# Optimization experiments

Measured on AMD Instinct MI355X. Metric: run time of the kernel, lower is better.

The kernel has to match this reference:

```python
import jax, jax.numpy as jnp
import numpy as np
import math

S, E = 4096, 2048
H = 4 * E  # FFN hidden
EPS = 1e-5


def _ln_all(y):
    # F.layer_norm(y, y.shape): normalize over ALL elements, no affine
    mu = jnp.mean(y)
    var = jnp.mean(jnp.square(y - mu))
    return (y - mu) / jnp.sqrt(var + EPS)


def setup_inputs() -> dict:
    key = jax.random.key(0)
    ks = jax.random.split(key, 12)
    sc = 0.02
    return {
        "x": jax.random.normal(ks[0], (S, E), dtype=jnp.float32),
        "Wq": jax.random.normal(ks[1], (E, E), dtype=jnp.float32) * sc,
        "bq": jnp.zeros((E,), dtype=jnp.float32),
        "Wk": jax.random.normal(ks[2], (E, E), dtype=jnp.float32) * sc,
        "bk": jnp.zeros((E,), dtype=jnp.float32),
        "Wv": jax.random.normal(ks[3], (E, E), dtype=jnp.float32) * sc,
        "bv": jnp.zeros((E,), dtype=jnp.float32),
        "W1": jax.random.normal(ks[4], (E, H), dtype=jnp.float32) * sc,
        "b1": jnp.zeros((H,), dtype=jnp.float32),
        "W2": jax.random.normal(ks[5], (H, E), dtype=jnp.float32) * sc,
        "b2": jnp.zeros((E,), dtype=jnp.float32),
    }


def reference(x, Wq, bq, Wk, bk, Wv, bv, W1, b1, W2, b2):
    # projections
    Q = x @ Wq + bq  # [S, E]
    K = x @ Wk + bk
    V = x @ Wv + bv
    # NOTE: source scales by sqrt(K.size(-2)) == sqrt(seq_len), not head dim
    scale = 1.0 / math.sqrt(x.shape[-2])
    scores = jax.nn.softmax((Q @ K.T) * scale, axis=-1)  # [S, S]
    attn = scores @ V  # [S, E]
    h = _ln_all(x + attn)
    ffn = jax.nn.relu(h @ W1 + b1) @ W2 + b2
    return _ln_all(h + ffn)
```

## Files before the change

kernel.cpp:

```cpp
#include <hip/hip_runtime.h>
#include <cstdint>
#include <cstddef>


constexpr int S = 4096;
constexpr int E = 2048;
constexpr int H = 8192;

typedef __bf16 bf16;
typedef bf16  bf16x8 __attribute__((ext_vector_type(8)));
typedef bf16  bf16x4 __attribute__((ext_vector_type(4)));
typedef float f32x4  __attribute__((ext_vector_type(4)));

typedef __attribute__((address_space(1))) void as1_void;
typedef __attribute__((address_space(3))) void as3_void;

__device__ __forceinline__ void ldg2lds16(const void* g, void* l) {
  __builtin_amdgcn_global_load_lds((as1_void*)g, (as3_void*)l, 16, 0, 0);
}

template <int EPI>
__global__ __launch_bounds__(256, 3)
void gemm_bt(const bf16* __restrict__ A, int lda,
             const bf16* __restrict__ Bt, int ldb,
             bf16* __restrict__ Cb, float* __restrict__ Cf, int ldc,
             const float* __restrict__ bias, const float* __restrict__ add,
             const bf16* __restrict__ addb,
             float* __restrict__ red, int M, int N, int K, float scale)
{
  __shared__ bf16 sA[128 * 64];
  __shared__ bf16 sB[128 * 64];

  const int tid  = threadIdx.x;
  const int lane = tid & 63;
  const int wave = tid >> 6;

  const int ntiles = gridDim.x;
  const int b      = blockIdx.y * ntiles + blockIdx.x;
  const int group  = b >> 6;
  const int within = b & 63;
  const int gpr    = ntiles >> 3;
  const int m0 = ((group / gpr) * 8 + (within >> 3)) * 128;
  const int n0 = ((group % gpr) * 8 + (within & 7)) * 128;

  const int wm = (wave & 1) * 64;
  const int wn = (wave >> 1) * 64;

  const int sr = tid >> 3;
  const int gsw = ((tid & 7) ^ (sr & 7)) * 8;
  const bf16* gA = A  + (size_t)(m0 + sr) * lda + gsw;
  const bf16* gB = Bt + (size_t)(n0 + sr) * ldb + gsw;
  const size_t a32 = (size_t)32 * lda;
  const size_t b32 = (size_t)32 * ldb;
  bf16* lA = &sA[tid * 8];
  bf16* lB = &sB[tid * 8];

  const int fr = lane & 15;
  const int fq = lane >> 4;
  const int p0 = (fq ^ (fr & 7)) * 8;
  const int p1 = p0 ^ 32;
  const bf16* rA = &sA[(wm + fr) * 64];
  const bf16* rB = &sB[(wn + fr) * 64];

  f32x4 acc[4][4] = {};

  for (int k0 = 0; k0 < K; k0 += 64) {
    ldg2lds16(gA,           lA);
    ldg2lds16(gA +     a32, lA + 32 * 64);
    ldg2lds16(gA + 2 * a32, lA + 64 * 64);
    ldg2lds16(gA + 3 * a32, lA + 96 * 64);
    ldg2lds16(gB,           lB);
    ldg2lds16(gB +     b32, lB + 32 * 64);
    ldg2lds16(gB + 2 * b32, lB + 64 * 64);
    ldg2lds16(gB + 3 * b32, lB + 96 * 64);
    gA += 64; gB += 64;
    __syncthreads();

    bf16x8 a0[4], a1[4], b0[4], b1[4];
#pragma unroll
    for (int i = 0; i < 4; ++i) {
      a0[i] = *(const bf16x8*)(rA + i * 1024 + p0);
      a1[i] = *(const bf16x8*)(rA + i * 1024 + p1);
    }
#pragma unroll
    for (int j = 0; j < 4; ++j) {
      b0[j] = *(const bf16x8*)(rB + j * 1024 + p0);
      b1[j] = *(const bf16x8*)(rB + j * 1024 + p1);
    }
#pragma unroll
    for (int i = 0; i < 4; ++i)
#pragma unroll
      for (int j = 0; j < 4; ++j)
        acc[i][j] = __builtin_amdgcn_mfma_f32_16x16x32_bf16(a0[i], b0[j], acc[i][j], 0, 0, 0);
#pragma unroll
    for (int i = 0; i < 4; ++i)
#pragma unroll
      for (int j = 0; j < 4; ++j)
        acc[i][j] = __builtin_amdgcn_mfma_f32_16x16x32_bf16(a1[i], b1[j], acc[i][j], 0, 0, 0);
    __syncthreads();
  }

  const int er = m0 + wm + fq * 4;
  const int ec = n0 + wn + fr;
  float ls = 0.f, ls2 = 0.f;
#pragma unroll
  for (int i = 0; i < 4; ++i) {
#pragma unroll
    for (int r = 0; r < 4; ++r) {
      const int gr = er + i * 16 + r;
#pragma unroll
      for (int j = 0; j < 4; ++j) {
        const int gc = ec + j * 16;
        const size_t idx = (size_t)gr * ldc + gc;
        float v = acc[i][j][r];
        if (EPI == 0) {
          v += bias[gc];
          Cb[idx] = (bf16)v;
        } else if (EPI == 1) {
          v += bias[gr];
          Cb[idx] = (bf16)v;
        } else if (EPI == 2) {
          Cb[idx] = (bf16)(v * scale);
        } else if (EPI == 3) {
          v += add[idx];
          Cf[idx] = v; ls += v; ls2 += v * v;
        } else if (EPI == 4) {
          v += bias[gc];
          v = v > 0.f ? v : 0.f;
          Cb[idx] = (bf16)v;
        } else {
          v += bias[gc] + (float)addb[idx];
          Cf[idx] = v; ls += v; ls2 += v * v;
        }
      }
    }
  }

  if (EPI == 3 || EPI == 5) {
#pragma unroll
    for (int o = 32; o; o >>= 1) {
      ls  += __shfl_xor(ls,  o, 64);
      ls2 += __shfl_xor(ls2, o, 64);
    }
    float* sred = (float*)sA;
    if (lane == 0) { sred[wave * 2] = ls; sred[wave * 2 + 1] = ls2; }
    __syncthreads();
    if (tid == 0) {
      atomicAdd(red,     sred[0] + sred[2] + sred[4] + sred[6]);
      atomicAdd(red + 1, sred[1] + sred[3] + sred[5] + sred[7]);
    }
  }
}

__global__ __launch_bounds__(256)
void cvt_f32_bf16(const float* __restrict__ src, bf16* __restrict__ dst)
{
  const size_t i = ((size_t)blockIdx.x * 256 + threadIdx.x) * 4;
  const float4 t = *(const float4*)(src + i);
  bf16x4 b;
  b[0] = (bf16)t.x; b[1] = (bf16)t.y; b[2] = (bf16)t.z; b[3] = (bf16)t.w;
  *(bf16x4*)(dst + i) = b;
}

__global__ __launch_bounds__(256)
void transpose_cvt(const float* __restrict__ src, bf16* __restrict__ dst, int R, int C)
{
  __shared__ float tile[32][33];
  const int c0 = blockIdx.x * 32, r0 = blockIdx.y * 32;
  const int tx = threadIdx.x & 31, ty = threadIdx.x >> 5;
#pragma unroll
  for (int rr = ty; rr < 32; rr += 8)
    tile[rr][tx] = src[(size_t)(r0 + rr) * C + (c0 + tx)];
  __syncthreads();
#pragma unroll
  for (int rr = ty; rr < 32; rr += 8)
    dst[(size_t)(c0 + rr) * R + (r0 + tx)] = (bf16)tile[tx][rr];
}

__global__ __launch_bounds__(256)
void softmax_rows(bf16* __restrict__ P)
{
  const int row  = blockIdx.x;
  bf16* p = P + (size_t)row * 4096;
  const int tid  = threadIdx.x;
  const int lane = tid & 63, wave = tid >> 6;

  bf16x8 c0 = *(const bf16x8*)(p + tid * 16);
  bf16x8 c1 = *(const bf16x8*)(p + tid * 16 + 8);
  float v[16];
#pragma unroll
  for (int i = 0; i < 8; ++i) { v[i] = (float)c0[i]; v[8 + i] = (float)c1[i]; }

  float m = v[0];
#pragma unroll
  for (int i = 1; i < 16; ++i) m = fmaxf(m, v[i]);
#pragma unroll
  for (int o = 32; o; o >>= 1) m = fmaxf(m, __shfl_xor(m, o, 64));
  __shared__ float sred[8];
  if (lane == 0) sred[wave] = m;
  __syncthreads();
  m = fmaxf(fmaxf(sred[0], sred[1]), fmaxf(sred[2], sred[3]));

  float s = 0.f;
#pragma unroll
  for (int i = 0; i < 16; ++i) { v[i] = __expf(v[i] - m); s += v[i]; }
#pragma unroll
  for (int o = 32; o; o >>= 1) s += __shfl_xor(s, o, 64);
  if (lane == 0) sred[4 + wave] = s;
  __syncthreads();
  s = sred[4] + sred[5] + sred[6] + sred[7];

  const float inv = 1.f / s;
  bf16x8 o0, o1;
#pragma unroll
  for (int i = 0; i < 8; ++i) { o0[i] = (bf16)(v[i] * inv); o1[i] = (bf16)(v[8 + i] * inv); }
  *(bf16x8*)(p + tid * 16)     = o0;
  *(bf16x8*)(p + tid * 16 + 8) = o1;
}

__global__ void ln_finalize(float* red, float n)
{
  const float mu  = red[0] / n;
  const float var = red[1] / n - mu * mu;
  red[2] = mu;
  red[3] = rsqrtf(var + 1e-5f);
}

__global__ __launch_bounds__(256)
void ln_apply(const float* __restrict__ y, const float* __restrict__ red,
              float* __restrict__ of, bf16* __restrict__ ob)
{
  const float mu = red[2], rs = red[3];
  const size_t i = ((size_t)blockIdx.x * 256 + threadIdx.x) * 4;
  float4 t = *(const float4*)(y + i);
  t.x = (t.x - mu) * rs; t.y = (t.y - mu) * rs;
  t.z = (t.z - mu) * rs; t.w = (t.w - mu) * rs;
  if (of) *(float4*)(of + i) = t;
  if (ob) {
    bf16x4 b;
    b[0] = (bf16)t.x; b[1] = (bf16)t.y; b[2] = (bf16)t.z; b[3] = (bf16)t.w;
    *(bf16x4*)(ob + i) = b;
  }
}

extern "C" void kernel_launch(void* const* d_in, const int* in_sizes, int n_in,
                              void* d_out, int out_size, void* d_ws, size_t ws_size,
                              hipStream_t stream)
{
  const float* x  = (const float*)d_in[0];
  const float* Wq = (const float*)d_in[1];
  const float* bq = (const float*)d_in[2];
  const float* Wk = (const float*)d_in[3];
  const float* bk = (const float*)d_in[4];
  const float* Wv = (const float*)d_in[5];
  const float* bv = (const float*)d_in[6];
  const float* W1 = (const float*)d_in[7];
  const float* b1 = (const float*)d_in[8];
  const float* W2 = (const float*)d_in[9];
  const float* b2 = (const float*)d_in[10];
  float* out = (float*)d_out;

  const size_t MB = 1ull << 20;
  char* ws = (char*)d_ws;

  bf16*  xb  = (bf16*)(ws);
  bf16*  hb  = xb;
  bf16*  WqT = (bf16*)(ws + 16 * MB);
  bf16*  WkT = (bf16*)(ws + 24 * MB);
  bf16*  WvT = (bf16*)(ws + 32 * MB);
  bf16*  W1T = (bf16*)(ws + 40 * MB);
  bf16*  W2T = (bf16*)(ws + 72 * MB);
  bf16*  Qb  = (bf16*)(ws + 104 * MB);
  bf16*  Kb  = (bf16*)(ws + 120 * MB);
  bf16*  Pb  = (bf16*)(ws + 136 * MB);
  bf16*  act = (bf16*)(ws + 104 * MB);
  bf16*  VbT = (bf16*)(ws + 168 * MB);
  float* y   = (float*)(ws + 184 * MB);
  float* red = (float*)(ws + 216 * MB);

  hipMemsetAsync(red, 0, 32, stream);

  const dim3 blk(256);
  const int nElemBlocks = (S * E) / 1024;

  cvt_f32_bf16<<<dim3(nElemBlocks), blk, 0, stream>>>(x, xb);
  transpose_cvt<<<dim3(E / 32, E / 32), blk, 0, stream>>>(Wq, WqT, E, E);
  transpose_cvt<<<dim3(E / 32, E / 32), blk, 0, stream>>>(Wk, WkT, E, E);
  transpose_cvt<<<dim3(E / 32, E / 32), blk, 0, stream>>>(Wv, WvT, E, E);
  transpose_cvt<<<dim3(H / 32, E / 32), blk, 0, stream>>>(W1, W1T, E, H);
  transpose_cvt<<<dim3(E / 32, H / 32), blk, 0, stream>>>(W2, W2T, H, E);

  gemm_bt<0><<<dim3(E / 128, S / 128), blk, 0, stream>>>(
      xb, E, WqT, E, Qb, nullptr, E, bq, nullptr, nullptr, nullptr, S, E, E, 0.f);
  gemm_bt<0><<<dim3(E / 128, S / 128), blk, 0, stream>>>(
      xb, E, WkT, E, Kb, nullptr, E, bk, nullptr, nullptr, nullptr, S, E, E, 0.f);
  gemm_bt<1><<<dim3(S / 128, E / 128), blk, 0, stream>>>(
      WvT, E, xb, E, VbT, nullptr, S, bv, nullptr, nullptr, nullptr, E, S, E, 0.f);

  gemm_bt<2><<<dim3(S / 128, S / 128), blk, 0, stream>>>(
      Qb, E, Kb, E, Pb, nullptr, S, nullptr, nullptr, nullptr, nullptr, S, S, E, 1.0f / 64.0f);
  softmax_rows<<<dim3(S), blk, 0, stream>>>(Pb);

  gemm_bt<3><<<dim3(E / 128, S / 128), blk, 0, stream>>>(
      Pb, S, VbT, S, nullptr, y, E, nullptr, x, nullptr, red, S, E, S, 0.f);
  ln_finalize<<<1, 1, 0, stream>>>(red, (float)((size_t)S * E));
  ln_apply<<<dim3(nElemBlocks), blk, 0, stream>>>(y, red, nullptr, hb);

  gemm_bt<4><<<dim3(H / 128, S / 128), blk, 0, stream>>>(
      hb, E, W1T, E, act, nullptr, H, b1, nullptr, nullptr, nullptr, S, H, E, 0.f);

  gemm_bt<5><<<dim3(E / 128, S / 128), blk, 0, stream>>>(
      act, H, W2T, H, nullptr, y, E, b2, nullptr, hb, red + 4, S, E, H, 0.f);
  ln_finalize<<<1, 1, 0, stream>>>(red + 4, (float)((size_t)S * E));
  ln_apply<<<dim3(nElemBlocks), blk, 0, stream>>>(y, red + 4, out, nullptr);
}
```

Baseline: 861.3 us.

## Replace GEMM with 8-wave 128x256 double-buffered pipelined kernel

Rewrites the bf16 GEMM used for all projections, attention, and FFN as a 512-thread, 128x256-tile kernel with double-buffered LDS. Global-to-LDS prefetches of the next K-slice are interleaved with four MFMA phases, using manual waitcnt, barriers and s_setprio. A new workgroup-to-tile remapping spreads consecutive block IDs. The aim is to hide global load latency and improve operand reuse. In exchange it uses more LDS and relies on fragile hand-placed synchronization.

New measurement: 1.005 ms. +16.7%, slower.

```diff
diff --git a/kernel.cpp b/kernel.cpp
--- a/kernel.cpp
+++ b/kernel.cpp
@@ -20,84 +20,151 @@
 }
 
 template <int EPI>
-__global__ __launch_bounds__(256, 3)
-void gemm_bt(const bf16* __restrict__ A, int lda,
-             const bf16* __restrict__ Bt, int ldb,
-             bf16* __restrict__ Cb, float* __restrict__ Cf, int ldc,
-             const float* __restrict__ bias, const float* __restrict__ add,
-             const bf16* __restrict__ addb,
-             float* __restrict__ red, int M, int N, int K, float scale)
-{
-  __shared__ bf16 sA[128 * 64];
-  __shared__ bf16 sB[128 * 64];
+__global__ __launch_bounds__(512, 2)
+void gemm8(const bf16* __restrict__ A, int lda,
+           const bf16* __restrict__ Bt, int ldb,
+           bf16* __restrict__ Cb, float* __restrict__ Cf, int ldc,
+           const float* __restrict__ bias, const float* __restrict__ add,
+           const bf16* __restrict__ addb,
+           float* __restrict__ red, int M, int N, int K, float scale)
+{
+  __shared__ bf16 sA[2][128 * 64];
+  __shared__ bf16 sB[2][256 * 64];
 
   const int tid  = threadIdx.x;
   const int lane = tid & 63;
   const int wave = tid >> 6;
 
-  const int ntiles = gridDim.x;
-  const int b      = blockIdx.y * ntiles + blockIdx.x;
-  const int group  = b >> 6;
-  const int within = b & 63;
-  const int gpr    = ntiles >> 3;
-  const int m0 = ((group / gpr) * 8 + (within >> 3)) * 128;
-  const int n0 = ((group % gpr) * 8 + (within & 7)) * 128;
+  const int nbx = gridDim.x;
+  const int nwg = nbx * gridDim.y;
+  const int bid = blockIdx.y * nbx + blockIdx.x;
+  const int wg  = (bid & 7) * (nwg >> 3) + (bid >> 3);
+  const int m0  = (wg / nbx) * 128;
+  const int n0  = (wg % nbx) * 256;
 
   const int wm = (wave & 1) * 64;
   const int wn = (wave >> 1) * 64;
 
-  const int sr = tid >> 3;
-  const int gsw = ((tid & 7) ^ (sr & 7)) * 8;
-  const bf16* gA = A  + (size_t)(m0 + sr) * lda + gsw;
-  const bf16* gB = Bt + (size_t)(n0 + sr) * ldb + gsw;
-  const size_t a32 = (size_t)32 * lda;
-  const size_t b32 = (size_t)32 * ldb;
-  bf16* lA = &sA[tid * 8];
-  bf16* lB = &sB[tid * 8];
+  const int tr  = tid >> 3;
+  const int tc  = tid & 7;
+  const int gsw = (tc ^ (tr & 7)) * 8;
+  const bf16* gA = A  + (size_t)(m0 + tr) * lda + gsw;
+  const bf16* gB = Bt + (size_t)(n0 + tr) * ldb + gsw;
+  const size_t a64 = (size_t)64 * lda;
+  const size_t b64 = (size_t)64 * ldb;
 
   const int fr = lane & 15;
   const int fq = lane >> 4;
   const int p0 = (fq ^ (fr & 7)) * 8;
   const int p1 = p0 ^ 32;
-  const bf16* rA = &sA[(wm + fr) * 64];
-  const bf16* rB = &sB[(wn + fr) * 64];
+
+  const int NT = K >> 6;
+
+  ldg2lds16(gA,             &sA[0][tid * 8]);
+  ldg2lds16(gA + a64,       &sA[0][4096  + tid * 8]);
+  ldg2lds16(gB,             &sB[0][tid * 8]);
+  ldg2lds16(gB + b64,       &sB[0][4096  + tid * 8]);
+  ldg2lds16(gB + 2 * b64,   &sB[0][8192  + tid * 8]);
+  ldg2lds16(gB + 3 * b64,   &sB[0][12288 + tid * 8]);
+  ldg2lds16(gA + 64,        &sA[1][tid * 8]);
+  ldg2lds16(gA + 64 + a64,  &sA[1][4096  + tid * 8]);
+  asm volatile("s_waitcnt vmcnt(2)" ::: "memory");
+  __builtin_amdgcn_s_barrier();
 
   f32x4 acc[4][4] = {};
 
-  for (int k0 = 0; k0 < K; k0 += 64) {
-    ldg2lds16(gA,           lA);
-    ldg2lds16(gA +     a32, lA + 32 * 64);
-    ldg2lds16(gA + 2 * a32, lA + 64 * 64);
-    ldg2lds16(gA + 3 * a32, lA + 96 * 64);
-    ldg2lds16(gB,           lB);
-    ldg2lds16(gB +     b32, lB + 32 * 64);
-    ldg2lds16(gB + 2 * b32, lB + 64 * 64);
-    ldg2lds16(gB + 3 * b32, lB + 96 * 64);
-    gA += 64; gB += 64;
-    __syncthreads();
-
-    bf16x8 a0[4], a1[4], b0[4], b1[4];
-#pragma unroll
-    for (int i = 0; i < 4; ++i) {
-      a0[i] = *(const bf16x8*)(rA + i * 1024 + p0);
-      a1[i] = *(const bf16x8*)(rA + i * 1024 + p1);
-    }
-#pragma unroll
-    for (int j = 0; j < 4; ++j) {
-      b0[j] = *(const bf16x8*)(rB + j * 1024 + p0);
-      b1[j] = *(const bf16x8*)(rB + j * 1024 + p1);
-    }
-#pragma unroll
-    for (int i = 0; i < 4; ++i)
-#pragma unroll
-      for (int j = 0; j < 4; ++j)
-        acc[i][j] = __builtin_amdgcn_mfma_f32_16x16x32_bf16(a0[i], b0[j], acc[i][j], 0, 0, 0);
-#pragma unroll
-    for (int i = 0; i < 4; ++i)
-#pragma unroll
-      for (int j = 0; j < 4; ++j)
-        acc[i][j] = __builtin_amdgcn_mfma_f32_16x16x32_bf16(a1[i], b1[j], acc[i][j], 0, 0, 0);
-    __syncthreads();
+  for (int t = 0; t < NT; ++t) {
+    const int bu = t & 1, nx = bu ^ 1;
+    const bf16* rA = &sA[bu][(wm + fr) * 64];
+    const bf16* rB = &sB[bu][(wn + fr) * 64];
+    bf16x8 aF0[2], aF1[2], bF0[4], bF1[4];
+
+    aF0[0] = *(const bf16x8*)(rA + p0);
+    aF1[0] = *(const bf16x8*)(rA + p1);
+    aF0[1] = *(const bf16x8*)(rA + 1024 + p0);
+    aF1[1] = *(const bf16x8*)(rA + 1024 + p1);
+    bF0[0] = *(const bf16x8*)(rB + p0);
+    bF1[0] = *(const bf16x8*)(rB + p1);
+    bF0[1] = *(const bf16x8*)(rB + 1024 + p0);
+    bF1[1] = *(const bf16x8*)(rB + 1024 + p1);
+    if (t + 1 < NT) {
+      const bf16* g = gB + ((size_t)(t + 1) << 6);
+      ldg2lds16(g,       &sB[nx][tid * 8]);
+      ldg2lds16(g + b64, &sB[nx][4096 + tid * 8]);
+    }
+    __builtin_amdgcn_s_barrier();
+    asm volatile("s_waitcnt lgkmcnt(0)" ::: "memory");
+    __builtin_amdgcn_s_setprio(1);
+#pragma unroll
+    for (int i = 0; i < 2; ++i)
+#pragma unroll
+      for (int j = 0; j < 2; ++j) {
+        acc[i][j] = __builtin_amdgcn_mfma_f32_16x16x32_bf16(aF0[i], bF0[j], acc[i][j], 0, 0, 0);
+        acc[i][j] = __builtin_amdgcn_mfma_f32_16x16x32_bf16(aF1[i], bF1[j], acc[i][j], 0, 0, 0);
+      }
+    __builtin_amdgcn_s_setprio(0);
+    __builtin_amdgcn_s_barrier();
+
+    bF0[2] = *(const bf16x8*)(rB + 2048 + p0);
+    bF1[2] = *(const bf16x8*)(rB + 2048 + p1);
+    bF0[3] = *(const bf16x8*)(rB + 3072 + p0);
+    bF1[3] = *(const bf16x8*)(rB + 3072 + p1);
+    if (t + 1 < NT) {
+      const bf16* g = gB + ((size_t)(t + 1) << 6) + 2 * b64;
+      ldg2lds16(g,       &sB[nx][8192  + tid * 8]);
+      ldg2lds16(g + b64, &sB[nx][12288 + tid * 8]);
+    }
+    __builtin_amdgcn_s_barrier();
+    asm volatile("s_waitcnt lgkmcnt(0)" ::: "memory");
+    __builtin_amdgcn_s_setprio(1);
+#pragma unroll
+    for (int i = 0; i < 2; ++i)
+#pragma unroll
+      for (int j = 0; j < 2; ++j) {
+        acc[i][2 + j] = __builtin_amdgcn_mfma_f32_16x16x32_bf16(aF0[i], bF0[2 + j], acc[i][2 + j], 0, 0, 0);
+        acc[i][2 + j] = __builtin_amdgcn_mfma_f32_16x16x32_bf16(aF1[i], bF1[2 + j], acc[i][2 + j], 0, 0, 0);
+      }
+    __builtin_amdgcn_s_setprio(0);
+    __builtin_amdgcn_s_barrier();
+
+    aF0[0] = *(const bf16x8*)(rA + 2048 + p0);
+    aF1[0] = *(const bf16x8*)(rA + 2048 + p1);
+    aF0[1] = *(const bf16x8*)(rA + 3072 + p0);
+    aF1[1] = *(const bf16x8*)(rA + 3072 + p1);
+    __builtin_amdgcn_s_barrier();
+    asm volatile("s_waitcnt lgkmcnt(0)" ::: "memory");
+    __builtin_amdgcn_s_setprio(1);
+#pragma unroll
+    for (int i = 0; i < 2; ++i)
+#pragma unroll
+      for (int j = 0; j < 2; ++j) {
+        acc[2 + i][j] = __builtin_amdgcn_mfma_f32_16x16x32_bf16(aF0[i], bF0[j], acc[2 + i][j], 0, 0, 0);
+        acc[2 + i][j] = __builtin_amdgcn_mfma_f32_16x16x32_bf16(aF1[i], bF1[j], acc[2 + i][j], 0, 0, 0);
+      }
+    __builtin_amdgcn_s_setprio(0);
+    __builtin_amdgcn_s_barrier();
+
+    if (t + 2 < NT) {
+      const bf16* g = gA + ((size_t)(t + 2) << 6);
+      ldg2lds16(g,       &sA[bu][tid * 8]);
+      ldg2lds16(g + a64, &sA[bu][4096 + tid * 8]);
+    }
+    __builtin_amdgcn_s_barrier();
+    __builtin_amdgcn_s_setprio(1);
+#pragma unroll
+    for (int i = 0; i < 2; ++i)
+#pragma unroll
+      for (int j = 0; j < 2; ++j) {
+        acc[2 + i][2 + j] = __builtin_amdgcn_mfma_f32_16x16x32_bf16(aF0[i], bF0[2 + j], acc[2 + i][2 + j], 0, 0, 0);
+        acc[2 + i][2 + j] = __builtin_amdgcn_mfma_f32_16x16x32_bf16(aF1[i], bF1[2 + j], acc[2 + i][2 + j], 0, 0, 0);
+      }
+    __builtin_amdgcn_s_setprio(0);
+    if (t + 2 < NT) {
+      asm volatile("s_waitcnt vmcnt(2)" ::: "memory");
+    } else {
+      asm volatile("s_waitcnt vmcnt(0)" ::: "memory");
+    }
+    __builtin_amdgcn_s_barrier();
   }
 
   const int er = m0 + wm + fq * 4;
@@ -146,8 +213,11 @@
     if (lane == 0) { sred[wave * 2] = ls; sred[wave * 2 + 1] = ls2; }
     __syncthreads();
     if (tid == 0) {
-      atomicAdd(red,     sred[0] + sred[2] + sred[4] + sred[6]);
-      atomicAdd(red + 1, sred[1] + sred[3] + sred[5] + sred[7]);
+      float a = 0.f, b = 0.f;
+#pragma unroll
+      for (int w = 0; w < 8; ++w) { a += sred[w * 2]; b += sred[w * 2 + 1]; }
+      atomicAdd(red,     a);
+      atomicAdd(red + 1, b);
     }
   }
 }
@@ -281,6 +351,7 @@
   hipMemsetAsync(red, 0, 32, stream);
 
   const dim3 blk(256);
+  const dim3 blkg(512);
   const int nElemBlocks = (S * E) / 1024;
 
   cvt_f32_bf16<<<dim3(nElemBlocks), blk, 0, stream>>>(x, xb);
@@ -290,26 +361,26 @@
   transpose_cvt<<<dim3(H / 32, E / 32), blk, 0, stream>>>(W1, W1T, E, H);
   transpose_cvt<<<dim3(E / 32, H / 32), blk, 0, stream>>>(W2, W2T, H, E);
 
-  gemm_bt<0><<<dim3(E / 128, S / 128), blk, 0, stream>>>(
+  gemm8<0><<<dim3(E / 256, S / 128), blkg, 0, stream>>>(
       xb, E, WqT, E, Qb, nullptr, E, bq, nullptr, nullptr, nullptr, S, E, E, 0.f);
-  gemm_bt<0><<<dim3(E / 128, S / 128), blk, 0, stream>>>(
+  gemm8<0><<<dim3(E / 256, S / 128), blkg, 0, stream>>>(
       xb, E, WkT, E, Kb, nullptr, E, bk, nullptr, nullptr, nullptr, S, E, E, 0.f);
-  gemm_bt<1><<<dim3(S / 128, E / 128), blk, 0, stream>>>(
+  gemm8<1><<<dim3(S / 256, E / 128), blkg, 0, stream>>>(
       WvT, E, xb, E, VbT, nullptr, S, bv, nullptr, nullptr, nullptr, E, S, E, 0.f);
 
-  gemm_bt<2><<<dim3(S / 128, S / 128), blk, 0, stream>>>(
+  gemm8<2><<<dim3(S / 256, S / 128), blkg, 0, stream>>>(
       Qb, E, Kb, E, Pb, nullptr, S, nullptr, nullptr, nullptr, nullptr, S, S, E, 1.0f / 64.0f);
   softmax_rows<<<dim3(S), blk, 0, stream>>>(Pb);
 
-  gemm_bt<3><<<dim3(E / 128, S / 128), blk, 0, stream>>>(
+  gemm8<3><<<dim3(E / 256, S / 128), blkg, 0, stream>>>(
       Pb, S, VbT, S, nullptr, y, E, nullptr, x, nullptr, red, S, E, S, 0.f);
   ln_finalize<<<1, 1, 0, stream>>>(red, (float)((size_t)S * E));
   ln_apply<<<dim3(nElemBlocks), blk, 0, stream>>>(y, red, nullptr, hb);
 
-  gemm_bt<4><<<dim3(H / 128, S / 128), blk, 0, stream>>>(
+  gemm8<4><<<dim3(H / 256, S / 128), blkg, 0, stream>>>(
       hb, E, W1T, E, act, nullptr, H, b1, nullptr, nullptr, nullptr, S, H, E, 0.f);
 
-  gemm_bt<5><<<dim3(E / 128, S / 128), blk, 0, stream>>>(
+  gemm8<5><<<dim3(E / 256, S / 128), blkg, 0, stream>>>(
       act, H, W2T, H, nullptr, y, E, b2, nullptr, hb, red + 4, S, E, H, 0.f);
   ln_finalize<<<1, 1, 0, stream>>>(red + 4, (float)((size_t)S * E));
   ln_apply<<<dim3(nElemBlocks), blk, 0, stream>>>(y, red + 4, out, nullptr);
```

## Add 256x256 double-buffered MFMA GEMM and fuse Q/K projections

Applied to the files above, without the earlier changes.

Adds a new 512-thread GEMM kernel with 256x256 output tiles, double-buffered LDS staging via global_load_lds, XOR-swizzled layout, workgroup remapping across XCDs, and interleaved loads and MFMAs with setprio. It replaces the Q and K projections with one fused GEMM over a concatenated weight and bias, and also uses the new kernel for QK^T and FFN1. The larger tiles raise data reuse per loaded byte and cut launch count. In exchange they use more LDS and registers, lower occupancy, and produce fewer workgroups, which may leave some CUs underfilled.

Measured after the change: 881.0 us. 1.02x slower.

```diff
diff --git a/kernel.cpp b/kernel.cpp
--- a/kernel.cpp
+++ b/kernel.cpp
@@ -17,6 +17,182 @@
 
 __device__ __forceinline__ void ldg2lds16(const void* g, void* l) {
   __builtin_amdgcn_global_load_lds((as1_void*)g, (as3_void*)l, 16, 0, 0);
+}
+
+template <int EPI>
+__global__ __launch_bounds__(512, 2)
+void gemm256(const bf16* __restrict__ A, int lda,
+             const bf16* __restrict__ Bt, int ldb,
+             bf16* __restrict__ Cb, int ldc,
+             const float* __restrict__ bias,
+             int M, int N, int K, float scale)
+{
+  __shared__ bf16 sA[2][256 * 64];
+  __shared__ bf16 sB[2][256 * 64];
+
+  const int tid  = threadIdx.x;
+  const int lane = tid & 63;
+  const int wave = tid >> 6;
+
+  const int nbx = gridDim.x;
+  const int nwg = nbx * gridDim.y;
+  const int bid = blockIdx.y * nbx + blockIdx.x;
+  const int wg  = (bid & 7) * (nwg >> 3) + (bid >> 3);
+  const int m0  = (wg / nbx) * 256;
+  const int n0  = (wg % nbx) * 256;
+
+  const int tr  = tid >> 3;
+  const int tc  = tid & 7;
+  const int gsw = (tc ^ (tr & 7)) * 8;
+  const bf16* gA = A  + (size_t)(m0 + tr) * lda + gsw;
+  const bf16* gB = Bt + (size_t)(n0 + tr) * ldb + gsw;
+  const size_t a64 = (size_t)64 * lda;
+  const size_t b64 = (size_t)64 * ldb;
+
+#define STAGE_A(t, g, b) ldg2lds16(gA + ((size_t)(t) << 6) + (size_t)(g) * a64, \
+                                   &sA[b][(g) * 4096 + tid * 8])
+#define STAGE_B(t, g, b) ldg2lds16(gB + ((size_t)(t) << 6) + (size_t)(g) * b64, \
+                                   &sB[b][(g) * 4096 + tid * 8])
+
+  const int fr = lane & 15;
+  const int fq = lane >> 4;
+  const int p0 = (fq ^ (fr & 7)) * 8;
+  const int p1 = p0 ^ 32;
+  const int wm = (wave & 1) * 128;
+  const int wn = (wave >> 1) * 64;
+
+  const int NT = K >> 6;
+
+  STAGE_A(0, 0, 0); STAGE_A(0, 1, 0); STAGE_A(0, 2, 0); STAGE_A(0, 3, 0);
+  STAGE_B(0, 0, 0); STAGE_B(0, 1, 0); STAGE_B(0, 2, 0); STAGE_B(0, 3, 0);
+  STAGE_A(1, 0, 1); STAGE_A(1, 2, 1);
+  STAGE_B(1, 0, 1); STAGE_B(1, 1, 1); STAGE_B(1, 2, 1); STAGE_B(1, 3, 1);
+  asm volatile("s_waitcnt vmcnt(6)" ::: "memory");
+  __builtin_amdgcn_s_barrier();
+
+  f32x4 acc[8][4] = {};
+
+#define KTILE(BU, NX, TT)                                                     \
+  {                                                                           \
+    const bf16* rA = &sA[BU][(wm + fr) * 64];                                 \
+    const bf16* rB = &sB[BU][(wn + fr) * 64];                                 \
+    bf16x8 a0[4], a1[4], bl0[2], bl1[2], bh0[2], bh1[2];                      \
+        \
+    _Pragma("unroll")                                                         \
+    for (int i = 0; i < 4; ++i) {                                             \
+      a0[i] = *(const bf16x8*)(rA + i * 1024 + p0);                           \
+      a1[i] = *(const bf16x8*)(rA + i * 1024 + p1);                           \
+    }                                                                         \
+    _Pragma("unroll")                                                         \
+    for (int j = 0; j < 2; ++j) {                                             \
+      bl0[j] = *(const bf16x8*)(rB + j * 1024 + p0);                          \
+      bl1[j] = *(const bf16x8*)(rB + j * 1024 + p1);                          \
+    }                                                                         \
+    if ((TT) + 1 < NT) { STAGE_A((TT) + 1, 1, NX); STAGE_A((TT) + 1, 3, NX); }\
+    __builtin_amdgcn_s_barrier();                                             \
+    asm volatile("s_waitcnt lgkmcnt(0)" ::: "memory");                        \
+    __builtin_amdgcn_s_setprio(1);                                            \
+    _Pragma("unroll")                                                         \
+    for (int i = 0; i < 4; ++i)                                               \
+      _Pragma("unroll")                                                       \
+      for (int j = 0; j < 2; ++j) {                                           \
+        acc[i][j] = __builtin_amdgcn_mfma_f32_16x16x32_bf16(a0[i], bl0[j], acc[i][j], 0, 0, 0); \
+        acc[i][j] = __builtin_amdgcn_mfma_f32_16x16x32_bf16(a1[i], bl1[j], acc[i][j], 0, 0, 0); \
+      }                                                                       \
+    __builtin_amdgcn_s_setprio(0);                                            \
+    __builtin_amdgcn_s_barrier();                                             \
+                \
+    _Pragma("unroll")                                                         \
+    for (int j = 0; j < 2; ++j) {                                             \
+      bh0[j] = *(const bf16x8*)(rB + (2 + j) * 1024 + p0);                    \
+      bh1[j] = *(const bf16x8*)(rB + (2 + j) * 1024 + p1);                    \
+    }                                                                         \
+    if ((TT) + 2 < NT) { STAGE_A((TT) + 2, 0, BU); STAGE_A((TT) + 2, 2, BU); }\
+    __builtin_amdgcn_s_barrier();                                             \
+    asm volatile("s_waitcnt lgkmcnt(0)" ::: "memory");                        \
+    __builtin_amdgcn_s_setprio(1);                                            \
+    _Pragma("unroll")                                                         \
+    for (int i = 0; i < 4; ++i)                                               \
+      _Pragma("unroll")                                                       \
+      for (int j = 0; j < 2; ++j) {                                           \
+        acc[i][2 + j] = __builtin_amdgcn_mfma_f32_16x16x32_bf16(a0[i], bh0[j], acc[i][2 + j], 0, 0, 0); \
+        acc[i][2 + j] = __builtin_amdgcn_mfma_f32_16x16x32_bf16(a1[i], bh1[j], acc[i][2 + j], 0, 0, 0); \
+      }                                                                       \
+    __builtin_amdgcn_s_setprio(0);                                            \
+    __builtin_amdgcn_s_barrier();                                             \
+                \
+    _Pragma("unroll")                                                         \
+    for (int i = 0; i < 4; ++i) {                                             \
+      a0[i] = *(const bf16x8*)(rA + 4096 + i * 1024 + p0);                    \
+      a1[i] = *(const bf16x8*)(rA + 4096 + i * 1024 + p1);                    \
+    }                                                                         \
+    if ((TT) + 2 < NT) { STAGE_B((TT) + 2, 0, BU); STAGE_B((TT) + 2, 1, BU); }\
+    __builtin_amdgcn_s_barrier();                                             \
+    asm volatile("s_waitcnt lgkmcnt(0)" ::: "memory");                        \
+    __builtin_amdgcn_s_setprio(1);                                            \
+    _Pragma("unroll")                                                         \
+    for (int i = 0; i < 4; ++i)                                               \
+      _Pragma("unroll")                                                       \
+      for (int j = 0; j < 2; ++j) {                                           \
+        acc[4 + i][2 + j] = __builtin_amdgcn_mfma_f32_16x16x32_bf16(a0[i], bh0[j], acc[4 + i][2 + j], 0, 0, 0); \
+        acc[4 + i][2 + j] = __builtin_amdgcn_mfma_f32_16x16x32_bf16(a1[i], bh1[j], acc[4 + i][2 + j], 0, 0, 0); \
+      }                                                                       \
+    __builtin_amdgcn_s_setprio(0);                                            \
+    __builtin_amdgcn_s_barrier();                                             \
+      \
+    if ((TT) + 2 < NT) { STAGE_B((TT) + 2, 2, BU); STAGE_B((TT) + 2, 3, BU); }\
+    __builtin_amdgcn_s_barrier();                                             \
+    __builtin_amdgcn_s_setprio(1);                                            \
+    _Pragma("unroll")                                                         \
+    for (int i = 0; i < 4; ++i)                                               \
+      _Pragma("unroll")                                                       \
+      for (int j = 0; j < 2; ++j) {                                           \
+        acc[4 + i][j] = __builtin_amdgcn_mfma_f32_16x16x32_bf16(a0[i], bl0[j], acc[4 + i][j], 0, 0, 0); \
+        acc[4 + i][j] = __builtin_amdgcn_mfma_f32_16x16x32_bf16(a1[i], bl1[j], acc[4 + i][j], 0, 0, 0); \
+      }                                                                       \
+    __builtin_amdgcn_s_setprio(0);                                            \
+    if ((TT) + 2 < NT) {                                                      \
+      asm volatile("s_waitcnt vmcnt(6)" ::: "memory");                        \
+    } else if ((TT) + 1 < NT) {                                               \
+      asm volatile("s_waitcnt vmcnt(0)" ::: "memory");                        \
+    }                                                                         \
+    __builtin_amdgcn_s_barrier();                                             \
+  }
+
+  for (int t = 0; t < NT; t += 2) {
+    KTILE(0, 1, t);
+    KTILE(1, 0, t + 1);
+  }
+#undef KTILE
+#undef STAGE_A
+#undef STAGE_B
+
+  const int er = m0 + wm + fq * 4;
+  const int ec = n0 + wn + fr;
+#pragma unroll
+  for (int qm = 0; qm < 2; ++qm) {
+#pragma unroll
+    for (int i = 0; i < 4; ++i) {
+#pragma unroll
+      for (int r = 0; r < 4; ++r) {
+        const int gr = er + qm * 64 + i * 16 + r;
+#pragma unroll
+        for (int j = 0; j < 4; ++j) {
+          const int gc = ec + j * 16;
+          const size_t idx = (size_t)gr * ldc + gc;
+          float v = acc[qm * 4 + i][j][r];
+          if (EPI == 0) {
+            Cb[idx] = (bf16)(v + bias[gc]);
+          } else if (EPI == 2) {
+            Cb[idx] = (bf16)(v * scale);
+          } else {
+            v += bias[gc];
+            Cb[idx] = (bf16)(v > 0.f ? v : 0.f);
+          }
+        }
+      }
+    }
+  }
 }
 
 template <int EPI>
@@ -178,6 +354,14 @@
 }
 
 __global__ __launch_bounds__(256)
+void concat_bias(const float* __restrict__ a, const float* __restrict__ b,
+                 float* __restrict__ o)
+{
+  const int i = blockIdx.x * 256 + threadIdx.x;
+  o[i] = (i < 2048) ? a[i] : b[i - 2048];
+}
+
+__global__ __launch_bounds__(256)
 void softmax_rows(bf16* __restrict__ P)
 {
   const int row  = blockIdx.x;
@@ -263,42 +447,42 @@
   const size_t MB = 1ull << 20;
   char* ws = (char*)d_ws;
 
-  bf16*  xb  = (bf16*)(ws);
-  bf16*  hb  = xb;
-  bf16*  WqT = (bf16*)(ws + 16 * MB);
-  bf16*  WkT = (bf16*)(ws + 24 * MB);
-  bf16*  WvT = (bf16*)(ws + 32 * MB);
-  bf16*  W1T = (bf16*)(ws + 40 * MB);
-  bf16*  W2T = (bf16*)(ws + 72 * MB);
-  bf16*  Qb  = (bf16*)(ws + 104 * MB);
-  bf16*  Kb  = (bf16*)(ws + 120 * MB);
-  bf16*  Pb  = (bf16*)(ws + 136 * MB);
-  bf16*  act = (bf16*)(ws + 104 * MB);
-  bf16*  VbT = (bf16*)(ws + 168 * MB);
-  float* y   = (float*)(ws + 184 * MB);
-  float* red = (float*)(ws + 216 * MB);
+  bf16*  xb   = (bf16*)(ws);
+  bf16*  hb   = xb;
+  bf16*  WqkT = (bf16*)(ws + 16 * MB);
+  bf16*  WvT  = (bf16*)(ws + 32 * MB);
+  bf16*  W1T  = (bf16*)(ws + 40 * MB);
+  bf16*  W2T  = (bf16*)(ws + 72 * MB);
+  bf16*  QKb  = (bf16*)(ws + 104 * MB);
+  bf16*  Pb   = (bf16*)(ws + 136 * MB);
+  bf16*  act  = (bf16*)(ws + 104 * MB);
+  bf16*  VbT  = (bf16*)(ws + 168 * MB);
+  float* y    = (float*)(ws + 184 * MB);
+  float* red  = (float*)(ws + 216 * MB);
+  float* bqk  = (float*)(ws + 216 * MB + 4096);
 
   hipMemsetAsync(red, 0, 32, stream);
 
   const dim3 blk(256);
+  const dim3 blkg(512);
   const int nElemBlocks = (S * E) / 1024;
 
   cvt_f32_bf16<<<dim3(nElemBlocks), blk, 0, stream>>>(x, xb);
-  transpose_cvt<<<dim3(E / 32, E / 32), blk, 0, stream>>>(Wq, WqT, E, E);
-  transpose_cvt<<<dim3(E / 32, E / 32), blk, 0, stream>>>(Wk, WkT, E, E);
+  transpose_cvt<<<dim3(E / 32, E / 32), blk, 0, stream>>>(Wq, WqkT, E, E);
+  transpose_cvt<<<dim3(E / 32, E / 32), blk, 0, stream>>>(Wk, WqkT + (size_t)E * E, E, E);
   transpose_cvt<<<dim3(E / 32, E / 32), blk, 0, stream>>>(Wv, WvT, E, E);
   transpose_cvt<<<dim3(H / 32, E / 32), blk, 0, stream>>>(W1, W1T, E, H);
   transpose_cvt<<<dim3(E / 32, H / 32), blk, 0, stream>>>(W2, W2T, H, E);
-
-  gemm_bt<0><<<dim3(E / 128, S / 128), blk, 0, stream>>>(
-      xb, E, WqT, E, Qb, nullptr, E, bq, nullptr, nullptr, nullptr, S, E, E, 0.f);
-  gemm_bt<0><<<dim3(E / 128, S / 128), blk, 0, stream>>>(
-      xb, E, WkT, E, Kb, nullptr, E, bk, nullptr, nullptr, nullptr, S, E, E, 0.f);
+  concat_bias<<<dim3(16), blk, 0, stream>>>(bq, bk, bqk);
+
+  gemm256<0><<<dim3(4096 / 256, S / 256), blkg, 0, stream>>>(
+      xb, E, WqkT, E, QKb, 4096, bqk, S, 4096, E, 0.f);
+
   gemm_bt<1><<<dim3(S / 128, E / 128), blk, 0, stream>>>(
       WvT, E, xb, E, VbT, nullptr, S, bv, nullptr, nullptr, nullptr, E, S, E, 0.f);
 
-  gemm_bt<2><<<dim3(S / 128, S / 128), blk, 0, stream>>>(
-      Qb, E, Kb, E, Pb, nullptr, S, nullptr, nullptr, nullptr, nullptr, S, S, E, 1.0f / 64.0f);
+  gemm256<2><<<dim3(S / 256, S / 256), blkg, 0, stream>>>(
+      QKb, 4096, QKb + 2048, 4096, Pb, S, nullptr, S, S, E, 1.0f / 64.0f);
   softmax_rows<<<dim3(S), blk, 0, stream>>>(Pb);
 
   gemm_bt<3><<<dim3(E / 128, S / 128), blk, 0, stream>>>(
@@ -306,8 +490,8 @@
   ln_finalize<<<1, 1, 0, stream>>>(red, (float)((size_t)S * E));
   ln_apply<<<dim3(nElemBlocks), blk, 0, stream>>>(y, red, nullptr, hb);
 
-  gemm_bt<4><<<dim3(H / 128, S / 128), blk, 0, stream>>>(
-      hb, E, W1T, E, act, nullptr, H, b1, nullptr, nullptr, nullptr, S, H, E, 0.f);
+  gemm256<4><<<dim3(H / 256, S / 256), blkg, 0, stream>>>(
+      hb, E, W1T, E, act, H, b1, S, H, E, 0.f);
 
   gemm_bt<5><<<dim3(E / 128, S / 128), blk, 0, stream>>>(
       act, H, W2T, H, nullptr, y, E, b2, nullptr, hb, red + 4, S, E, H, 0.f);
```
